# Optimization experiments

Hardware: AMD Instinct MI355X
Metric: run time of the kernel (lower is better)

The kernel has to match this reference:

```python
import jax, jax.numpy as jnp
import numpy as np

INPUT_DIM = 64
AUG_DIM = 64
HIDDEN = 256
BATCH = 4096
T = 50


def setup_inputs() -> dict:
    key = jax.random.key(0)
    k0, k1, k2 = jax.random.split(key, 3)
    D = INPUT_DIM + AUG_DIM
    x0 = jax.random.normal(k0, (BATCH, INPUT_DIM), jnp.float32)
    t = jnp.linspace(0.0, 1.0, T).astype(jnp.float32)
    W1 = jax.random.normal(k1, (D, HIDDEN), jnp.float32) / np.sqrt(D).astype(np.float32)
    b1 = jnp.zeros((HIDDEN,), jnp.float32)
    W2 = jax.random.normal(k2, (HIDDEN, D), jnp.float32) / np.sqrt(HIDDEN).astype(np.float32)
    b2 = jnp.zeros((D,), jnp.float32)
    return {"x0": x0, "t": t, "W1": W1, "b1": b1, "W2": W2, "b2": b2}


def reference(x0, t, W1, b1, W2, b2):
    # ode_func: time-independent MLP on the augmented state [B, D]
    def f(ti, y):
        return jnp.tanh(y @ W1 + b1) @ W2 + b2

    B = x0.shape[0]
    # augment with zeros -> [B, INPUT_DIM + AUG_DIM]
    y0 = jnp.concatenate([x0, jnp.zeros((B, AUG_DIM), x0.dtype)], axis=-1)

    # torchdiffeq 'rk4' fixed-grid solver: one 3/8-rule RK4 step per interval
    def step(y, ts):
        t0, t1 = ts
        dt = t1 - t0
        third = dt * (1.0 / 3.0)
        k1 = f(t0, y)
        k2 = f(t0 + third, y + third * k1)
        k3 = f(t0 + 2.0 * third, y + dt * (k2 - k1 * (1.0 / 3.0)))
        k4 = f(t1, y + dt * (k1 - k2 + k3))
        y1 = y + dt * 0.125 * (k1 + 3.0 * (k2 + k3) + k4)
        return y1, y1

    _, ys = jax.lax.scan(step, y0, (t[:-1], t[1:]))  # [T-1, B, D]
    sol = jnp.concatenate([y0[None], ys], axis=0)    # [T, B, D]
    return sol[..., :INPUT_DIM]                      # drop augmented dims
```

## Files before the change

kernel.cpp:

```cpp
#include <hip/hip_runtime.h>

typedef __attribute__((ext_vector_type(8))) _Float16 f16x8;
typedef __attribute__((ext_vector_type(4))) _Float16 f16x4;
typedef __attribute__((ext_vector_type(4))) float f32x4;

#define T_STEPS 49
#define BM 16
#define OUTSTRIDE (4096*64)
#define YSTR 132
#define HSTR 260

__device__ __forceinline__ float fast_tanh(float x) {
  float e = __builtin_amdgcn_exp2f(x * 2.885390081777927f);
  return 1.f - 2.f * __builtin_amdgcn_rcpf(e + 1.f);
}
__device__ __forceinline__ f16x8 ld_frag(const _Float16* p) {
  f16x4 a = *(const f16x4*)p;
  f16x4 b = *(const f16x4*)(p + 4);
  return __builtin_shufflevector(a, b, 0,1,2,3,4,5,6,7);
}

__global__ __launch_bounds__(512)
void node_rk4_kernel(const float* __restrict__ x0, const float* __restrict__ tarr,
                     const float* __restrict__ W1, const float* __restrict__ b1,
                     const float* __restrict__ W2, const float* __restrict__ b2,
                     float* __restrict__ out)
{
  __shared__ __align__(16) _Float16 Yh[16][YSTR];
  __shared__ __align__(16) _Float16 Hh[16][HSTR];

  const int tid  = threadIdx.x;
  const int w    = tid >> 6;
  const int lane = tid & 63;
  const int m    = lane & 15;
  const int g    = lane >> 4;
  const int row0 = (int)blockIdx.x * BM;
  const int col  = 16*w + m;

  f16x8 wB1[2][4], wB2[8];
#pragma unroll
  for (int tt = 0; tt < 2; ++tt)
#pragma unroll
    for (int kk = 0; kk < 4; ++kk) {
      f16x8 v;
#pragma unroll
      for (int j = 0; j < 8; ++j)
        v[j] = (_Float16)W1[(kk*32 + 8*g + j)*256 + (32*w + 16*tt + m)];
      wB1[tt][kk] = v;
    }
#pragma unroll
  for (int kk = 0; kk < 8; ++kk) {
    f16x8 v;
#pragma unroll
    for (int j = 0; j < 8; ++j)
      v[j] = (_Float16)W2[(kk*32 + 8*g + j)*128 + col];
    wB2[kk] = v;
  }
  const float bb1a = b1[32*w + m];
  const float bb1b = b1[32*w + 16 + m];
  const float bb2  = b2[col];

  float y[4], k1[4], k2[4], k3[4], yn[4];
#pragma unroll
  for (int i = 0; i < 4; ++i) {
    float v = (col < 64) ? x0[(row0 + 4*g + i)*64 + col] : 0.f;
    y[i] = v; yn[i] = v;
  }
  if (col < 64) {
#pragma unroll
    for (int i = 0; i < 4; ++i)
      out[(row0 + 4*g + i)*64 + col] = y[i];
  }

  for (int step = 0; step < T_STEPS; ++step) {
    const float dt = tarr[step+1] - tarr[step];
    const float third = dt * (1.f/3.f);

#pragma unroll
    for (int stage = 0; stage < 4; ++stage) {
#pragma unroll
      for (int i = 0; i < 4; ++i)
        Yh[4*g + i][col] = (_Float16)yn[i];
      __syncthreads();

      f32x4 acc0 = { bb1a, bb1a, bb1a, bb1a };
      f32x4 acc1 = { bb1b, bb1b, bb1b, bb1b };
#pragma unroll
      for (int kk = 0; kk < 4; ++kk) {
        f16x8 a = ld_frag(&Yh[m][kk*32 + 8*g]);
        acc0 = __builtin_amdgcn_mfma_f32_16x16x32_f16(a, wB1[0][kk], acc0, 0,0,0);
        acc1 = __builtin_amdgcn_mfma_f32_16x16x32_f16(a, wB1[1][kk], acc1, 0,0,0);
      }
#pragma unroll
      for (int i = 0; i < 4; ++i) {
        Hh[4*g + i][32*w + m]      = (_Float16)fast_tanh(acc0[i]);
        Hh[4*g + i][32*w + 16 + m] = (_Float16)fast_tanh(acc1[i]);
      }
      __syncthreads();

      f32x4 accA = { bb2, bb2, bb2, bb2 };
      f32x4 accB = { 0.f, 0.f, 0.f, 0.f };
#pragma unroll
      for (int kk = 0; kk < 4; ++kk) {
        f16x8 aA = ld_frag(&Hh[m][kk*32 + 8*g]);
        f16x8 aB = ld_frag(&Hh[m][(kk+4)*32 + 8*g]);
        accA = __builtin_amdgcn_mfma_f32_16x16x32_f16(aA, wB2[kk],   accA, 0,0,0);
        accB = __builtin_amdgcn_mfma_f32_16x16x32_f16(aB, wB2[kk+4], accB, 0,0,0);
      }

      if (stage == 0) {
#pragma unroll
        for (int i = 0; i < 4; ++i) { k1[i] = accA[i]+accB[i]; yn[i] = y[i] + third*k1[i]; }
      } else if (stage == 1) {
#pragma unroll
        for (int i = 0; i < 4; ++i) { k2[i] = accA[i]+accB[i]; yn[i] = y[i] + dt*(k2[i] - k1[i]*(1.f/3.f)); }
      } else if (stage == 2) {
#pragma unroll
        for (int i = 0; i < 4; ++i) { k3[i] = accA[i]+accB[i]; yn[i] = y[i] + dt*(k1[i] - k2[i] + k3[i]); }
      } else {
#pragma unroll
        for (int i = 0; i < 4; ++i) {
          float k4 = accA[i]+accB[i];
          y[i] += dt*0.125f*(k1[i] + 3.f*(k2[i]+k3[i]) + k4);
          yn[i] = y[i];
        }
        if (col < 64) {
#pragma unroll
          for (int i = 0; i < 4; ++i)
            out[(step+1)*OUTSTRIDE + (row0 + 4*g + i)*64 + col] = y[i];
        }
      }
    }
  }
}

extern "C" void kernel_launch(void* const* d_in, const int* in_sizes, int n_in,
                              void* d_out, int out_size, void* d_ws, size_t ws_size,
                              hipStream_t stream) {
  const float* x0 = (const float*)d_in[0];
  const float* t  = (const float*)d_in[1];
  const float* W1 = (const float*)d_in[2];
  const float* b1 = (const float*)d_in[3];
  const float* W2 = (const float*)d_in[4];
  const float* b2 = (const float*)d_in[5];
  float* out = (float*)d_out;
  hipLaunchKernelGGL(node_rk4_kernel, dim3(4096/BM), dim3(512), 0, stream,
                     x0, t, W1, b1, W2, b2, out);
}
```

Measured before the change: 166.0 us.

## Halve block to four waves, each computing twice the output columns

Shrinks each block from 8 to 4 waves. Each wave now owns 64 hidden columns in the first GEMM and 32 state columns in the second, so it issues more MFMAs per synchronization and shares each A-fragment load across more tiles. It also asks for 2 blocks per CU through launch bounds, and computes dt with an inline-asm subtract. The trade-off is roughly twice the weight registers per thread and fewer waves per block available to hide barrier latency.

```diff
diff --git a/kernel.cpp b/kernel.cpp
--- a/kernel.cpp
+++ b/kernel.cpp
@@ -19,8 +19,13 @@
   f16x4 b = *(const f16x4*)(p + 4);
   return __builtin_shufflevector(a, b, 0,1,2,3,4,5,6,7);
 }
+__device__ __forceinline__ float vsub(float a, float b) {
+  float r;
+  asm("v_sub_f32 %0, %1, %2" : "=v"(r) : "v"(a), "v"(b));
+  return r;
+}
 
-__global__ __launch_bounds__(512)
+__global__ __launch_bounds__(256, 2)
 void node_rk4_kernel(const float* __restrict__ x0, const float* __restrict__ tarr,
                      const float* __restrict__ W1, const float* __restrict__ b1,
                      const float* __restrict__ W2, const float* __restrict__ b2,
@@ -35,99 +40,131 @@
   const int m    = lane & 15;
   const int g    = lane >> 4;
   const int row0 = (int)blockIdx.x * BM;
-  const int col  = 16*w + m;
 
-  f16x8 wB1[2][4], wB2[8];
+  f16x8 wB1[4][4];
+  f16x8 wB2[2][8];
 #pragma unroll
-  for (int tt = 0; tt < 2; ++tt)
+  for (int t = 0; t < 4; ++t)
 #pragma unroll
     for (int kk = 0; kk < 4; ++kk) {
       f16x8 v;
 #pragma unroll
       for (int j = 0; j < 8; ++j)
-        v[j] = (_Float16)W1[(kk*32 + 8*g + j)*256 + (32*w + 16*tt + m)];
-      wB1[tt][kk] = v;
+        v[j] = (_Float16)W1[(kk*32 + 8*g + j)*256 + (64*w + 16*t + m)];
+      wB1[t][kk] = v;
     }
 #pragma unroll
-  for (int kk = 0; kk < 8; ++kk) {
-    f16x8 v;
+  for (int t = 0; t < 2; ++t)
 #pragma unroll
-    for (int j = 0; j < 8; ++j)
-      v[j] = (_Float16)W2[(kk*32 + 8*g + j)*128 + col];
-    wB2[kk] = v;
-  }
-  const float bb1a = b1[32*w + m];
-  const float bb1b = b1[32*w + 16 + m];
-  const float bb2  = b2[col];
+    for (int kk = 0; kk < 8; ++kk) {
+      f16x8 v;
+#pragma unroll
+      for (int j = 0; j < 8; ++j)
+        v[j] = (_Float16)W2[(kk*32 + 8*g + j)*128 + (32*w + 16*t + m)];
+      wB2[t][kk] = v;
+    }
+  float bb1[4], bb2[2];
+#pragma unroll
+  for (int t = 0; t < 4; ++t) bb1[t] = b1[64*w + 16*t + m];
+#pragma unroll
+  for (int t = 0; t < 2; ++t) bb2[t] = b2[32*w + 16*t + m];
 
-  float y[4], k1[4], k2[4], k3[4], yn[4];
+  const int c0 = 32*w + m;
+  const int c1 = c0 + 16;
+
+  float y[2][4], k1[2][4], k2[2][4], k3[2][4], yn[2][4];
 #pragma unroll
   for (int i = 0; i < 4; ++i) {
-    float v = (col < 64) ? x0[(row0 + 4*g + i)*64 + col] : 0.f;
-    y[i] = v; yn[i] = v;
+    float v0 = (c0 < 64) ? x0[(row0 + 4*g + i)*64 + c0] : 0.f;
+    float v1 = (c1 < 64) ? x0[(row0 + 4*g + i)*64 + c1] : 0.f;
+    y[0][i] = v0; yn[0][i] = v0;
+    y[1][i] = v1; yn[1][i] = v1;
   }
-  if (col < 64) {
+  if (c0 < 64) {
 #pragma unroll
-    for (int i = 0; i < 4; ++i)
-      out[(row0 + 4*g + i)*64 + col] = y[i];
+    for (int i = 0; i < 4; ++i) {
+      out[(row0 + 4*g + i)*64 + c0] = y[0][i];
+      out[(row0 + 4*g + i)*64 + c1] = y[1][i];
+    }
   }
 
   for (int step = 0; step < T_STEPS; ++step) {
-    const float dt = tarr[step+1] - tarr[step];
+    const float dt = vsub(tarr[step+1], tarr[step]);
     const float third = dt * (1.f/3.f);
 
 #pragma unroll
     for (int stage = 0; stage < 4; ++stage) {
 #pragma unroll
-      for (int i = 0; i < 4; ++i)
-        Yh[4*g + i][col] = (_Float16)yn[i];
+      for (int i = 0; i < 4; ++i) {
+        Yh[4*g + i][c0] = (_Float16)yn[0][i];
+        Yh[4*g + i][c1] = (_Float16)yn[1][i];
+      }
       __syncthreads();
 
-      f32x4 acc0 = { bb1a, bb1a, bb1a, bb1a };
-      f32x4 acc1 = { bb1b, bb1b, bb1b, bb1b };
+      f32x4 acc[4];
+#pragma unroll
+      for (int t = 0; t < 4; ++t) acc[t] = (f32x4){ bb1[t], bb1[t], bb1[t], bb1[t] };
 #pragma unroll
       for (int kk = 0; kk < 4; ++kk) {
         f16x8 a = ld_frag(&Yh[m][kk*32 + 8*g]);
-        acc0 = __builtin_amdgcn_mfma_f32_16x16x32_f16(a, wB1[0][kk], acc0, 0,0,0);
-        acc1 = __builtin_amdgcn_mfma_f32_16x16x32_f16(a, wB1[1][kk], acc1, 0,0,0);
+#pragma unroll
+        for (int t = 0; t < 4; ++t)
+          acc[t] = __builtin_amdgcn_mfma_f32_16x16x32_f16(a, wB1[t][kk], acc[t], 0,0,0);
       }
 #pragma unroll
-      for (int i = 0; i < 4; ++i) {
-        Hh[4*g + i][32*w + m]      = (_Float16)fast_tanh(acc0[i]);
-        Hh[4*g + i][32*w + 16 + m] = (_Float16)fast_tanh(acc1[i]);
-      }
+      for (int t = 0; t < 4; ++t)
+#pragma unroll
+        for (int i = 0; i < 4; ++i)
+          Hh[4*g + i][64*w + 16*t + m] = (_Float16)fast_tanh(acc[t][i]);
       __syncthreads();
 
-      f32x4 accA = { bb2, bb2, bb2, bb2 };
-      f32x4 accB = { 0.f, 0.f, 0.f, 0.f };
+      f32x4 accA[2], accB[2];
+#pragma unroll
+      for (int t = 0; t < 2; ++t) {
+        accA[t] = (f32x4){ bb2[t], bb2[t], bb2[t], bb2[t] };
+        accB[t] = (f32x4){ 0.f, 0.f, 0.f, 0.f };
+      }
 #pragma unroll
       for (int kk = 0; kk < 4; ++kk) {
         f16x8 aA = ld_frag(&Hh[m][kk*32 + 8*g]);
         f16x8 aB = ld_frag(&Hh[m][(kk+4)*32 + 8*g]);
-        accA = __builtin_amdgcn_mfma_f32_16x16x32_f16(aA, wB2[kk],   accA, 0,0,0);
-        accB = __builtin_amdgcn_mfma_f32_16x16x32_f16(aB, wB2[kk+4], accB, 0,0,0);
+#pragma unroll
+        for (int t = 0; t < 2; ++t) {
+          accA[t] = __builtin_amdgcn_mfma_f32_16x16x32_f16(aA, wB2[t][kk],   accA[t], 0,0,0);
+          accB[t] = __builtin_amdgcn_mfma_f32_16x16x32_f16(aB, wB2[t][kk+4], accB[t], 0,0,0);
+        }
       }
 
       if (stage == 0) {
 #pragma unroll
-        for (int i = 0; i < 4; ++i) { k1[i] = accA[i]+accB[i]; yn[i] = y[i] + third*k1[i]; }
+        for (int t = 0; t < 2; ++t)
+#pragma unroll
+          for (int i = 0; i < 4; ++i) { k1[t][i] = accA[t][i]+accB[t][i]; yn[t][i] = y[t][i] + third*k1[t][i]; }
       } else if (stage == 1) {
 #pragma unroll
-        for (int i = 0; i < 4; ++i) { k2[i] = accA[i]+accB[i]; yn[i] = y[i] + dt*(k2[i] - k1[i]*(1.f/3.f)); }
+        for (int t = 0; t < 2; ++t)
+#pragma unroll
+          for (int i = 0; i < 4; ++i) { k2[t][i] = accA[t][i]+accB[t][i]; yn[t][i] = y[t][i] + dt*(k2[t][i] - k1[t][i]*(1.f/3.f)); }
       } else if (stage == 2) {
 #pragma unroll
-        for (int i = 0; i < 4; ++i) { k3[i] = accA[i]+accB[i]; yn[i] = y[i] + dt*(k1[i] - k2[i] + k3[i]); }
+        for (int t = 0; t < 2; ++t)
+#pragma unroll
+          for (int i = 0; i < 4; ++i) { k3[t][i] = accA[t][i]+accB[t][i]; yn[t][i] = y[t][i] + dt*(k1[t][i] - k2[t][i] + k3[t][i]); }
       } else {
 #pragma unroll
-        for (int i = 0; i < 4; ++i) {
-          float k4 = accA[i]+accB[i];
-          y[i] += dt*0.125f*(k1[i] + 3.f*(k2[i]+k3[i]) + k4);
-          yn[i] = y[i];
-        }
-        if (col < 64) {
+        for (int t = 0; t < 2; ++t)
 #pragma unroll
-          for (int i = 0; i < 4; ++i)
-            out[(step+1)*OUTSTRIDE + (row0 + 4*g + i)*64 + col] = y[i];
+          for (int i = 0; i < 4; ++i) {
+            float k4 = accA[t][i]+accB[t][i];
+            y[t][i] += dt*0.125f*(k1[t][i] + 3.f*(k2[t][i]+k3[t][i]) + k4);
+            yn[t][i] = y[t][i];
+          }
+        if (c0 < 64) {
+#pragma unroll
+          for (int i = 0; i < 4; ++i) {
+            out[(step+1)*OUTSTRIDE + (row0 + 4*g + i)*64 + c0] = y[0][i];
+            out[(step+1)*OUTSTRIDE + (row0 + 4*g + i)*64 + c1] = y[1][i];
+          }
         }
       }
     }
@@ -144,6 +181,6 @@
   const float* W2 = (const float*)d_in[4];
   const float* b2 = (const float*)d_in[5];
   float* out = (float*)d_out;
-  hipLaunchKernelGGL(node_rk4_kernel, dim3(4096/BM), dim3(512), 0, stream,
+  hipLaunchKernelGGL(node_rk4_kernel, dim3(4096/BM), dim3(256), 0, stream,
                      x0, t, W1, b1, W2, b2, out);
 }
```

Result: slower. 210.5 us (+26.8%).

## Swap MFMA operands to transpose output layout for vectorized LDS and global stores

Applied to the files above, without the earlier changes.

The MFMA operand order is swapped so each lane holds four consecutive columns of one row instead of four rows of one column. Shared-memory writes of Y and H become packed f16x4 stores, and global loads and stores of the state become float4 accesses. The Y writeback is moved to the end of each stage with the barrier after it. An inline-asm subtract keeps dt from being folded. The intent is fewer LDS and global memory instructions per stage, at the cost of reworked indexing for biases and state.

```diff
diff --git a/kernel.cpp b/kernel.cpp
--- a/kernel.cpp
+++ b/kernel.cpp
@@ -19,6 +19,11 @@
   f16x4 b = *(const f16x4*)(p + 4);
   return __builtin_shufflevector(a, b, 0,1,2,3,4,5,6,7);
 }
+__device__ __forceinline__ float vsub(float a, float b) {
+  float r;
+  asm("v_sub_f32 %0, %1, %2" : "=v"(r) : "v"(a), "v"(b));
+  return r;
+}
 
 __global__ __launch_bounds__(512)
 void node_rk4_kernel(const float* __restrict__ x0, const float* __restrict__ tarr,
@@ -35,77 +40,86 @@
   const int m    = lane & 15;
   const int g    = lane >> 4;
   const int row0 = (int)blockIdx.x * BM;
-  const int col  = 16*w + m;
 
   f16x8 wB1[2][4], wB2[8];
 #pragma unroll
-  for (int tt = 0; tt < 2; ++tt)
+  for (int c = 0; c < 2; ++c)
 #pragma unroll
     for (int kk = 0; kk < 4; ++kk) {
       f16x8 v;
 #pragma unroll
       for (int j = 0; j < 8; ++j)
-        v[j] = (_Float16)W1[(kk*32 + 8*g + j)*256 + (32*w + 16*tt + m)];
-      wB1[tt][kk] = v;
+        v[j] = (_Float16)W1[(kk*32 + 8*g + j)*256 + (32*w + 16*c + m)];
+      wB1[c][kk] = v;
     }
 #pragma unroll
   for (int kk = 0; kk < 8; ++kk) {
     f16x8 v;
 #pragma unroll
     for (int j = 0; j < 8; ++j)
-      v[j] = (_Float16)W2[(kk*32 + 8*g + j)*128 + col];
+      v[j] = (_Float16)W2[(kk*32 + 8*g + j)*128 + (16*w + m)];
     wB2[kk] = v;
   }
-  const float bb1a = b1[32*w + m];
-  const float bb1b = b1[32*w + 16 + m];
-  const float bb2  = b2[col];
+  f32x4 bb1[2], bb2v;
+#pragma unroll
+  for (int c = 0; c < 2; ++c)
+#pragma unroll
+    for (int i = 0; i < 4; ++i) bb1[c][i] = b1[16*(2*w + c) + 4*g + i];
+#pragma unroll
+  for (int i = 0; i < 4; ++i) bb2v[i] = b2[16*w + 4*g + i];
 
+  const int ccol = 16*w + 4*g;
   float y[4], k1[4], k2[4], k3[4], yn[4];
+  if (ccol < 64) {
+    const float4 v = *(const float4*)&x0[(row0 + m)*64 + ccol];
+    y[0]=v.x; y[1]=v.y; y[2]=v.z; y[3]=v.w;
+  } else {
+    y[0]=y[1]=y[2]=y[3]=0.f;
+  }
 #pragma unroll
-  for (int i = 0; i < 4; ++i) {
-    float v = (col < 64) ? x0[(row0 + 4*g + i)*64 + col] : 0.f;
-    y[i] = v; yn[i] = v;
+  for (int i = 0; i < 4; ++i) yn[i] = y[i];
+  if (ccol < 64) {
+    float4 v; v.x=y[0]; v.y=y[1]; v.z=y[2]; v.w=y[3];
+    *(float4*)&out[(row0 + m)*64 + ccol] = v;
   }
-  if (col < 64) {
+  {
+    f16x4 p;
 #pragma unroll
-    for (int i = 0; i < 4; ++i)
-      out[(row0 + 4*g + i)*64 + col] = y[i];
+    for (int i = 0; i < 4; ++i) p[i] = (_Float16)yn[i];
+    *(f16x4*)&Yh[m][ccol] = p;
   }
+  __syncthreads();
 
   for (int step = 0; step < T_STEPS; ++step) {
-    const float dt = tarr[step+1] - tarr[step];
+    const float dt = vsub(tarr[step+1], tarr[step]);
     const float third = dt * (1.f/3.f);
 
 #pragma unroll
     for (int stage = 0; stage < 4; ++stage) {
-#pragma unroll
-      for (int i = 0; i < 4; ++i)
-        Yh[4*g + i][col] = (_Float16)yn[i];
-      __syncthreads();
-
-      f32x4 acc0 = { bb1a, bb1a, bb1a, bb1a };
-      f32x4 acc1 = { bb1b, bb1b, bb1b, bb1b };
+      f32x4 acc0 = bb1[0], acc1 = bb1[1];
 #pragma unroll
       for (int kk = 0; kk < 4; ++kk) {
         f16x8 a = ld_frag(&Yh[m][kk*32 + 8*g]);
-        acc0 = __builtin_amdgcn_mfma_f32_16x16x32_f16(a, wB1[0][kk], acc0, 0,0,0);
-        acc1 = __builtin_amdgcn_mfma_f32_16x16x32_f16(a, wB1[1][kk], acc1, 0,0,0);
+        acc0 = __builtin_amdgcn_mfma_f32_16x16x32_f16(wB1[0][kk], a, acc0, 0,0,0);
+        acc1 = __builtin_amdgcn_mfma_f32_16x16x32_f16(wB1[1][kk], a, acc1, 0,0,0);
       }
+      {
+        f16x4 p0, p1;
 #pragma unroll
-      for (int i = 0; i < 4; ++i) {
-        Hh[4*g + i][32*w + m]      = (_Float16)fast_tanh(acc0[i]);
-        Hh[4*g + i][32*w + 16 + m] = (_Float16)fast_tanh(acc1[i]);
+        for (int i = 0; i < 4; ++i) { p0[i] = (_Float16)fast_tanh(acc0[i]); p1[i] = (_Float16)fast_tanh(acc1[i]); }
+        *(f16x4*)&Hh[m][16*(2*w+0) + 4*g] = p0;
+        *(f16x4*)&Hh[m][16*(2*w+1) + 4*g] = p1;
       }
       __syncthreads();
 
-      f32x4 accA = { bb2, bb2, bb2, bb2 };
+      f32x4 accA = bb2v;
       f32x4 accB = { 0.f, 0.f, 0.f, 0.f };
 #pragma unroll
       for (int kk = 0; kk < 4; ++kk) {
         f16x8 aA = ld_frag(&Hh[m][kk*32 + 8*g]);
         f16x8 aB = ld_frag(&Hh[m][(kk+4)*32 + 8*g]);
-        accA = __builtin_amdgcn_mfma_f32_16x16x32_f16(aA, wB2[kk],   accA, 0,0,0);
-        accB = __builtin_amdgcn_mfma_f32_16x16x32_f16(aB, wB2[kk+4], accB, 0,0,0);
+        accA = __builtin_amdgcn_mfma_f32_16x16x32_f16(wB2[kk],   aA, accA, 0,0,0);
+        accB = __builtin_amdgcn_mfma_f32_16x16x32_f16(wB2[kk+4], aB, accB, 0,0,0);
       }
 
       if (stage == 0) {
@@ -124,12 +138,18 @@
           y[i] += dt*0.125f*(k1[i] + 3.f*(k2[i]+k3[i]) + k4);
           yn[i] = y[i];
         }
-        if (col < 64) {
-#pragma unroll
-          for (int i = 0; i < 4; ++i)
-            out[(step+1)*OUTSTRIDE + (row0 + 4*g + i)*64 + col] = y[i];
+        if (ccol < 64) {
+          float4 v; v.x=y[0]; v.y=y[1]; v.z=y[2]; v.w=y[3];
+          *(float4*)&out[(size_t)(step+1)*OUTSTRIDE + (row0 + m)*64 + ccol] = v;
         }
       }
+      {
+        f16x4 p;
+#pragma unroll
+        for (int i = 0; i < 4; ++i) p[i] = (_Float16)yn[i];
+        *(f16x4*)&Yh[m][ccol] = p;
+      }
+      __syncthreads();
     }
   }
 }
```

Result: faster. 151.6 us (-8.6%).
